# Optimization experiments

Hardware: AMD Instinct MI355X
Metric: run time of the kernel (lower is better)

Reference implementation:

```python
import jax, jax.numpy as jnp
import numpy as np

B, T, D = 8, 1024, 1024
H = 16
DH = D // H  # 64


def setup_inputs() -> dict:
    key = jax.random.key(0)
    k1, k2, k3 = jax.random.split(key, 3)
    x = jax.random.normal(k1, (B, T, D), dtype=jnp.float32)
    W_qkv = jax.random.normal(k2, (3 * D, D), dtype=jnp.float32) * (D ** -0.5)
    W_proj = jax.random.normal(k3, (D, D), dtype=jnp.float32) * (D ** -0.5)
    return {"x": x, "W_qkv": W_qkv, "W_proj": W_proj}


def reference(x, W_qkv, W_proj):
    b, t, _ = x.shape
    # qkv: [B,T,3*D] -> [B,T,3,H,DH]
    qkv = (x @ W_qkv.T).reshape(b, t, 3, H, DH)
    q, k, v = qkv[:, :, 0], qkv[:, :, 1], qkv[:, :, 2]  # [B,T,H,DH]
    scale = DH ** -0.5
    # scores: [B,H,Tq,Tk]
    scores = jnp.einsum("bqhd,bkhd->bhqk", q, k) * scale
    # NOTE: softmax over dim=-2 (the QUERY axis), as in the original module
    attn = jax.nn.softmax(scores, axis=-2)
    out = jnp.einsum("bhqk,bkhd->bqhd", attn, v).reshape(b, t, D)
    return out @ W_proj.T
```

## Files before the change

### kernel.cpp

```cpp
#include <hip/hip_runtime.h>


typedef __bf16 bf16_t;
typedef __bf16 bf16x8 __attribute__((ext_vector_type(8)));
typedef __bf16 bf16x4 __attribute__((ext_vector_type(4)));
typedef float f32x4 __attribute__((ext_vector_type(4)));
typedef unsigned short u16x8 __attribute__((ext_vector_type(8)));
typedef short s16x4 __attribute__((ext_vector_type(4)));

#define DEV __device__ __forceinline__
#define C2 0.18033688f

DEV void gld_lds16(const bf16_t* g, bf16_t* l) {
  __builtin_amdgcn_global_load_lds(
      (const __attribute__((address_space(1))) unsigned int*)g,
      (__attribute__((address_space(3))) unsigned int*)l, 16, 0, 0);
}

DEV float exp2c(float x) { return __builtin_amdgcn_exp2f(fminf(x, 30.f)); }
DEV float sanit(float v) { return (v == v) ? fminf(fmaxf(v, -1e4f), 1e4f) : 0.f; }

DEV int sw64(int r, int kc) { return r * 64 + (((kc ^ (r + (r >> 3))) & 7) << 3); }
DEV int sw32(int r, int kc) { return r * 32 + (((kc ^ r ^ (r >> 2)) & 3) << 3); }

DEV f32x4 mfma16(bf16x8 a, bf16x8 b, f32x4 c) {
  return __builtin_amdgcn_mfma_f32_16x16x32_bf16(a, b, c, 0, 0, 0);
}

DEV f32x4 mfma16k16(bf16x4 a, bf16x4 b, f32x4 c) {
#if defined(__has_builtin) && __has_builtin(__builtin_amdgcn_mfma_f32_16x16x16bf16_1k)
  union U { bf16x4 h; s16x4 s; };
  U ua, ub;
  ua.h = a;
  ub.h = b;
  return __builtin_amdgcn_mfma_f32_16x16x16bf16_1k(ua.s, ub.s, c, 0, 0, 0);
#else
  f32x4 d;
  asm("v_mfma_f32_16x16x16_bf16 %0, %1, %2, %3"
      : "=v"(d)
      : "v"(a), "v"(b), "v"(c));
  return d;
#endif
}

DEV bf16x4 lo4(bf16x8 v) { return __builtin_shufflevector(v, v, 0, 1, 2, 3); }
DEV bf16x4 hi4(bf16x8 v) { return __builtin_shufflevector(v, v, 4, 5, 6, 7); }

__global__ void detect_dtype(const unsigned short* x, int* flag) {
  __shared__ int smax;
  if (threadIdx.x == 0) smax = 0;
  __syncthreads();
  int m = 0;
  for (int i = threadIdx.x; i < 16384; i += 256) {
    int e = (x[i] >> 7) & 0xFF;
    m = m > e ? m : e;
  }
  atomicMax(&smax, m);
  __syncthreads();
  if (threadIdx.x == 0) *flag = (smax >= 160) ? 1 : 0;
}

__global__ void convert_in(const void* __restrict__ x, const void* __restrict__ wq,
                           const void* __restrict__ wp, bf16_t* __restrict__ xb,
                           bf16_t* __restrict__ wqb, bf16_t* __restrict__ wpb,
                           const int* __restrict__ flag) {
  int i = blockIdx.x * 256 + threadIdx.x;
  const void* src;
  bf16_t* dst;
  int off;
  if (i < 1048576) { src = x; dst = xb; off = i; }
  else if (i < 1441792) { src = wq; dst = wqb; off = i - 1048576; }
  else { src = wp; dst = wpb; off = i - 1441792; }
  if (*flag) {
    const float4* s = (const float4*)src;
    float4 a = s[off * 2], b = s[off * 2 + 1];
    bf16x8 o;
    o[0] = (bf16_t)a.x; o[1] = (bf16_t)a.y; o[2] = (bf16_t)a.z; o[3] = (bf16_t)a.w;
    o[4] = (bf16_t)b.x; o[5] = (bf16_t)b.y; o[6] = (bf16_t)b.z; o[7] = (bf16_t)b.w;
    *(bf16x8*)(dst + (size_t)off * 8) = o;
  } else {
    ((u16x8*)dst)[off] = ((const u16x8*)src)[off];
  }
}

__global__ __launch_bounds__(256, 2)
void gemm_bt(const bf16_t* __restrict__ A, int lda, const bf16_t* __restrict__ B,
             bf16_t* __restrict__ Cb, float* __restrict__ Cf, int ldc,
             int K, const int* __restrict__ f32flag) {
  __shared__ bf16_t sA[128 * 32];
  __shared__ bf16_t sB[128 * 32];
  const int tid = threadIdx.x;
  const int wave = tid >> 6, lane = tid & 63;
  const int l = lane & 15, quad = lane >> 4;
  const int row0 = blockIdx.y * 128, col0 = blockIdx.x * 128;
  const int wm = (wave >> 1) * 64, wn = (wave & 1) * 64;
  f32x4 acc[4][4];
#pragma unroll
  for (int i = 0; i < 4; ++i)
#pragma unroll
    for (int j = 0; j < 4; ++j) acc[i][j] = f32x4{0.f, 0.f, 0.f, 0.f};

  for (int k0 = 0; k0 < K; k0 += 32) {
    __syncthreads();
#pragma unroll
    for (int t = 0; t < 2; ++t) {
      int base = t * 256 + wave * 64;
      int n = base + lane;
      int r = n >> 2;
      int kc = ((n & 3) ^ r ^ (r >> 2)) & 3;
      gld_lds16(A + (size_t)(row0 + r) * lda + k0 + kc * 8, sA + base * 8);
      gld_lds16(B + (size_t)(col0 + r) * K + k0 + kc * 8, sB + base * 8);
    }
    __syncthreads();
    bf16x8 af[4], bfr[4];
#pragma unroll
    for (int i = 0; i < 4; ++i)
      af[i] = *(const bf16x8*)&sA[sw32(wm + i * 16 + l, quad)];
#pragma unroll
    for (int j = 0; j < 4; ++j)
      bfr[j] = *(const bf16x8*)&sB[sw32(wn + j * 16 + l, quad)];
#pragma unroll
    for (int i = 0; i < 4; ++i)
#pragma unroll
      for (int j = 0; j < 4; ++j)
        acc[i][j] = mfma16(af[i], bfr[j], acc[i][j]);
  }
  const bool of32 = (f32flag != nullptr) && (*f32flag != 0);
#pragma unroll
  for (int i = 0; i < 4; ++i) {
    int rr = row0 + wm + i * 16 + quad * 4;
#pragma unroll
    for (int j = 0; j < 4; ++j) {
      int cc = col0 + wn + j * 16 + l;
#pragma unroll
      for (int t = 0; t < 4; ++t) {
        float v = sanit(acc[i][j][t]);
        size_t idx = (size_t)(rr + t) * ldc + cc;
        if (of32) Cf[idx] = v; else Cb[idx] = (bf16_t)v;
      }
    }
  }
}

__global__ __launch_bounds__(256, 4)
void attn_stats(const bf16_t* __restrict__ qkv, bf16_t* __restrict__ Vts) {
  __shared__ bf16_t sK[128 * 64];
  __shared__ bf16_t sV[128 * 64];
  __shared__ float sL[128];
  const int bh = blockIdx.x, kt = blockIdx.y;
  const int b = bh >> 4, h = bh & 15;
  const int tid = threadIdx.x, wave = tid >> 6, lane = tid & 63;
  const int l = lane & 15, quad = lane >> 4;
  const size_t rowK = (size_t)b * 1024 + kt * 128;

#pragma unroll
  for (int t = 0; t < 4; ++t) {
    int base = wave * 256 + t * 64;
    int n = base + lane;
    int r = n >> 3;
    int kc = ((n & 7) ^ (r + (r >> 3))) & 7;
    gld_lds16(qkv + (rowK + r) * 3072 + 2048 + h * 64 + kc * 8, sV + base * 8);
    gld_lds16(qkv + (rowK + r) * 3072 + 1024 + h * 64 + kc * 8, sK + base * 8);
  }
  if (tid < 128) sL[tid] = 0.f;
  __syncthreads();

  float accj[8];
#pragma unroll
  for (int j = 0; j < 8; ++j) accj[j] = 0.f;

  for (int qt = 0; qt < 8; ++qt) {
    bf16x8 aq[2][2];
#pragma unroll
    for (int i = 0; i < 2; ++i)
#pragma unroll
      for (int ks = 0; ks < 2; ++ks)
        aq[i][ks] = *(const bf16x8*)&qkv[((size_t)b * 1024 + qt * 128 + wave * 32 +
                                          i * 16 + l) * 3072 + h * 64 +
                                         (ks * 4 + quad) * 8];
#pragma unroll
    for (int j = 0; j < 8; ++j) {
      f32x4 s0 = {0.f, 0.f, 0.f, 0.f}, s1 = {0.f, 0.f, 0.f, 0.f};
#pragma unroll
      for (int ks = 0; ks < 2; ++ks) {
        bf16x8 bk = *(const bf16x8*)&sK[sw64(j * 16 + l, ks * 4 + quad)];
        s0 = mfma16(aq[0][ks], bk, s0);
        s1 = mfma16(aq[1][ks], bk, s1);
      }
#pragma unroll
      for (int t = 0; t < 4; ++t)
        accj[j] += exp2c(s0[t] * C2) + exp2c(s1[t] * C2);
    }
  }
#pragma unroll
  for (int j = 0; j < 8; ++j) {
    float v = accj[j];
    v += __shfl_xor(v, 16);
    v += __shfl_xor(v, 32);
    if (lane < 16) atomicAdd(&sL[j * 16 + l], v);
  }
  __syncthreads();
  if (tid < 128) sL[tid] = 1.0f / fmaxf(sL[tid], 1e-20f);
  __syncthreads();

#pragma unroll
  for (int t = 0; t < 4; ++t) {
    int u = t * 256 + tid;
    int d = u >> 4, k0 = (u & 15) * 8;
    bf16x8 pk;
#pragma unroll
    for (int i = 0; i < 8; ++i) {
      int kl = (k0 & ~31) | ((i >> 2) << 4) | (((k0 >> 3) & 3) << 2) | (i & 3);
      float v = (float)sV[sw64(kl, d >> 3) + (d & 7)];
      pk[i] = (bf16_t)(v * sL[kl]);
    }
    *(bf16x8*)&Vts[((size_t)bh * 64 + d) * 1024 + kt * 128 + k0] = pk;
  }
}

__global__ __launch_bounds__(256, 4)
void attn_out_k(const bf16_t* __restrict__ qkv, const bf16_t* __restrict__ Vts,
                bf16_t* __restrict__ attn) {
  __shared__ bf16_t sK[2][128 * 64];
  const int bh = blockIdx.x, qt = blockIdx.y;
  const int b = bh >> 4, h = bh & 15;
  const int tid = threadIdx.x, wave = tid >> 6, lane = tid & 63;
  const int l = lane & 15, quad = lane >> 4;
  const bf16_t* qbase = qkv + (size_t)b * 3145728 + h * 64;
  const bf16_t* vbase = Vts + (size_t)bh * 65536;

  bf16x8 bq[2][2];
#pragma unroll
  for (int i = 0; i < 2; ++i)
#pragma unroll
    for (int ks = 0; ks < 2; ++ks)
      bq[i][ks] = *(const bf16x8*)&qbase[(size_t)(qt * 128 + wave * 32 + i * 16 + l) *
                                             3072 + ks * 32 + quad * 8];
  f32x4 o[2][4];
#pragma unroll
  for (int i = 0; i < 2; ++i)
#pragma unroll
    for (int jd = 0; jd < 4; ++jd) o[i][jd] = f32x4{0.f, 0.f, 0.f, 0.f};

#pragma unroll
  for (int t = 0; t < 4; ++t) {
    int base = wave * 256 + t * 64;
    int n = base + lane;
    int r = n >> 3;
    int kc = ((n & 7) ^ (r + (r >> 3))) & 7;
    gld_lds16(qkv + ((size_t)b * 1024 + r) * 3072 + 1024 + h * 64 + kc * 8,
              sK[0] + base * 8);
  }

  for (int kt = 0; kt < 8; ++kt) {
    const int buf = kt & 1;
    __syncthreads();
    if (kt < 7) {
#pragma unroll
      for (int t = 0; t < 4; ++t) {
        int base = wave * 256 + t * 64;
        int n = base + lane;
        int r = n >> 3;
        int kc = ((n & 7) ^ (r + (r >> 3))) & 7;
        gld_lds16(qkv + ((size_t)b * 1024 + (kt + 1) * 128 + r) * 3072 + 1024 +
                      h * 64 + kc * 8,
                  sK[buf ^ 1] + base * 8);
      }
    }
    const bf16_t* sKb = sK[buf];
    const bf16_t* vcol = vbase + kt * 128;

    bf16x8 va[2][4];
#pragma unroll
    for (int pc = 0; pc < 2; ++pc)
#pragma unroll
      for (int jd = 0; jd < 4; ++jd)
        va[pc][jd] = *(const bf16x8*)&vcol[(size_t)(jd * 16 + l) * 1024 +
                                           pc * 32 + quad * 8];

#pragma unroll
    for (int ch = 0; ch < 4; ++ch) {
      const int cur = ch & 1;
      bf16x8 ak[2][2];
#pragma unroll
      for (int kk = 0; kk < 2; ++kk)
#pragma unroll
        for (int ks = 0; ks < 2; ++ks)
          ak[kk][ks] = *(const bf16x8*)&sKb[sw64(ch * 32 + kk * 16 + l,
                                                 ks * 4 + quad)];
#pragma unroll
      for (int i = 0; i < 2; ++i) {
        f32x4 st0 = {0.f, 0.f, 0.f, 0.f}, st1 = {0.f, 0.f, 0.f, 0.f};
        st0 = mfma16(ak[0][0], bq[i][0], st0);
        st0 = mfma16(ak[0][1], bq[i][1], st0);
        st1 = mfma16(ak[1][0], bq[i][0], st1);
        st1 = mfma16(ak[1][1], bq[i][1], st1);
        bf16x4 p0, p1;
#pragma unroll
        for (int t = 0; t < 4; ++t) {
          p0[t] = (bf16_t)exp2c(st0[t] * C2);
          p1[t] = (bf16_t)exp2c(st1[t] * C2);
        }
#pragma unroll
        for (int jd = 0; jd < 4; ++jd) {
          o[i][jd] = mfma16k16(lo4(va[cur][jd]), p0, o[i][jd]);
          o[i][jd] = mfma16k16(hi4(va[cur][jd]), p1, o[i][jd]);
        }
      }
      if (ch < 2) {
#pragma unroll
        for (int jd = 0; jd < 4; ++jd)
          va[cur][jd] = *(const bf16x8*)&vcol[(size_t)(jd * 16 + l) * 1024 +
                                              (ch + 2) * 32 + quad * 8];
      }
    }
  }
#pragma unroll
  for (int i = 0; i < 2; ++i) {
    size_t row = (size_t)b * 1024 + qt * 128 + wave * 32 + i * 16 + l;
#pragma unroll
    for (int jd = 0; jd < 4; ++jd) {
      bf16x4 pk;
#pragma unroll
      for (int t = 0; t < 4; ++t) pk[t] = (bf16_t)sanit(o[i][jd][t]);
      *(bf16x4*)&attn[row * 3072 + h * 64 + jd * 16 + quad * 4] = pk;
    }
  }
}

extern "C" void kernel_launch(void* const* d_in, const int* in_sizes, int n_in,
                              void* d_out, int out_size, void* d_ws, size_t ws_size,
                              hipStream_t stream) {
  (void)in_sizes; (void)n_in; (void)out_size; (void)ws_size;
  char* w = (char*)d_ws;
  bf16_t* qkv = (bf16_t*)w;
  bf16_t* xb = (bf16_t*)(w + 50331648);
  bf16_t* Vts = xb;
  bf16_t* Wqkvb = (bf16_t*)(w + 67108864);
  bf16_t* Wprojb = (bf16_t*)(w + 73400320);
  int* flag = (int*)(w + 75497472);
  bf16_t* attn = qkv + 2048;

  detect_dtype<<<1, 256, 0, stream>>>((const unsigned short*)d_in[0], flag);
  convert_in<<<6144, 256, 0, stream>>>(d_in[0], d_in[1], d_in[2],
                                       xb, Wqkvb, Wprojb, flag);

  gemm_bt<<<dim3(24, 64), 256, 0, stream>>>(xb, 1024, Wqkvb, qkv, nullptr, 3072,
                                            1024, nullptr);
  attn_stats<<<dim3(128, 8), 256, 0, stream>>>(qkv, Vts);
  attn_out_k<<<dim3(128, 8), 256, 0, stream>>>(qkv, Vts, attn);
  gemm_bt<<<dim3(8, 64), 256, 0, stream>>>(attn, 3072, Wprojb, (bf16_t*)d_out,
                                           (float*)d_out, 1024, 1024, flag);
}
```

Before: 320.3 us.

## Stage V tiles in LDS and double query tile per attention block

The attention-output kernel now runs 512 threads per block covering 256 query rows instead of 128, which halves the grid. It also stages the pre-scaled transposed V tile into a swizzled, double-buffered LDS array with async global-to-LDS loads, replacing the direct per-wave global reads of V. This lets more query rows share each K/V tile load and cuts redundant global V traffic. The cost is doubled LDS per block (about 64KB) and fewer blocks, which may limit occupancy and latency hiding.

After: 296.1 us. 7.6% less time.

```diff
diff --git a/kernel.cpp b/kernel.cpp
--- a/kernel.cpp
+++ b/kernel.cpp
@@ -218,10 +218,11 @@
   }
 }
 
-__global__ __launch_bounds__(256, 4)
+__global__ __launch_bounds__(512, 4)
 void attn_out_k(const bf16_t* __restrict__ qkv, const bf16_t* __restrict__ Vts,
                 bf16_t* __restrict__ attn) {
   __shared__ bf16_t sK[2][128 * 64];
+  __shared__ bf16_t sV[2][64 * 128];
   const int bh = blockIdx.x, qt = blockIdx.y;
   const int b = bh >> 4, h = bh & 15;
   const int tid = threadIdx.x, wave = tid >> 6, lane = tid & 63;
@@ -234,7 +235,7 @@
   for (int i = 0; i < 2; ++i)
 #pragma unroll
     for (int ks = 0; ks < 2; ++ks)
-      bq[i][ks] = *(const bf16x8*)&qbase[(size_t)(qt * 128 + wave * 32 + i * 16 + l) *
+      bq[i][ks] = *(const bf16x8*)&qbase[(size_t)(qt * 256 + wave * 32 + i * 16 + l) *
                                              3072 + ks * 32 + quad * 8];
   f32x4 o[2][4];
 #pragma unroll
@@ -243,13 +244,15 @@
     for (int jd = 0; jd < 4; ++jd) o[i][jd] = f32x4{0.f, 0.f, 0.f, 0.f};
 
 #pragma unroll
-  for (int t = 0; t < 4; ++t) {
-    int base = wave * 256 + t * 64;
-    int n = base + lane;
+  for (int t = 0; t < 2; ++t) {
+    int n = t * 512 + tid;
     int r = n >> 3;
     int kc = ((n & 7) ^ (r + (r >> 3))) & 7;
     gld_lds16(qkv + ((size_t)b * 1024 + r) * 3072 + 1024 + h * 64 + kc * 8,
-              sK[0] + base * 8);
+              sK[0] + n * 8);
+    int d = n >> 4, s = n & 15;
+    int c = s ^ (d & 7);
+    gld_lds16(vbase + (size_t)d * 1024 + c * 8, sV[0] + n * 8);
   }
 
   for (int kt = 0; kt < 8; ++kt) {
@@ -257,30 +260,24 @@
     __syncthreads();
     if (kt < 7) {
 #pragma unroll
-      for (int t = 0; t < 4; ++t) {
-        int base = wave * 256 + t * 64;
-        int n = base + lane;
+      for (int t = 0; t < 2; ++t) {
+        int n = t * 512 + tid;
         int r = n >> 3;
         int kc = ((n & 7) ^ (r + (r >> 3))) & 7;
         gld_lds16(qkv + ((size_t)b * 1024 + (kt + 1) * 128 + r) * 3072 + 1024 +
                       h * 64 + kc * 8,
-                  sK[buf ^ 1] + base * 8);
+                  sK[buf ^ 1] + n * 8);
+        int d = n >> 4, s = n & 15;
+        int c = s ^ (d & 7);
+        gld_lds16(vbase + (size_t)d * 1024 + (kt + 1) * 128 + c * 8,
+                  sV[buf ^ 1] + n * 8);
       }
     }
     const bf16_t* sKb = sK[buf];
-    const bf16_t* vcol = vbase + kt * 128;
-
-    bf16x8 va[2][4];
-#pragma unroll
-    for (int pc = 0; pc < 2; ++pc)
-#pragma unroll
-      for (int jd = 0; jd < 4; ++jd)
-        va[pc][jd] = *(const bf16x8*)&vcol[(size_t)(jd * 16 + l) * 1024 +
-                                           pc * 32 + quad * 8];
+    const bf16_t* sVb = sV[buf];
 
 #pragma unroll
     for (int ch = 0; ch < 4; ++ch) {
-      const int cur = ch & 1;
       bf16x8 ak[2][2];
 #pragma unroll
       for (int kk = 0; kk < 2; ++kk)
@@ -288,6 +285,11 @@
         for (int ks = 0; ks < 2; ++ks)
           ak[kk][ks] = *(const bf16x8*)&sKb[sw64(ch * 32 + kk * 16 + l,
                                                  ks * 4 + quad)];
+      bf16x8 va[4];
+#pragma unroll
+      for (int jd = 0; jd < 4; ++jd)
+        va[jd] = *(const bf16x8*)&sVb[(jd * 16 + l) * 128 +
+                                      (((ch * 4 + quad) ^ (l & 7)) << 3)];
 #pragma unroll
       for (int i = 0; i < 2; ++i) {
         f32x4 st0 = {0.f, 0.f, 0.f, 0.f}, st1 = {0.f, 0.f, 0.f, 0.f};
@@ -303,21 +305,15 @@
         }
 #pragma unroll
         for (int jd = 0; jd < 4; ++jd) {
-          o[i][jd] = mfma16k16(lo4(va[cur][jd]), p0, o[i][jd]);
-          o[i][jd] = mfma16k16(hi4(va[cur][jd]), p1, o[i][jd]);
+          o[i][jd] = mfma16k16(lo4(va[jd]), p0, o[i][jd]);
+          o[i][jd] = mfma16k16(hi4(va[jd]), p1, o[i][jd]);
         }
       }
-      if (ch < 2) {
-#pragma unroll
-        for (int jd = 0; jd < 4; ++jd)
-          va[cur][jd] = *(const bf16x8*)&vcol[(size_t)(jd * 16 + l) * 1024 +
-                                              (ch + 2) * 32 + quad * 8];
-      }
     }
   }
 #pragma unroll
   for (int i = 0; i < 2; ++i) {
-    size_t row = (size_t)b * 1024 + qt * 128 + wave * 32 + i * 16 + l;
+    size_t row = (size_t)b * 1024 + qt * 256 + wave * 32 + i * 16 + l;
 #pragma unroll
     for (int jd = 0; jd < 4; ++jd) {
       bf16x4 pk;
@@ -348,7 +344,7 @@
   gemm_bt<<<dim3(24, 64), 256, 0, stream>>>(xb, 1024, Wqkvb, qkv, nullptr, 3072,
                                             1024, nullptr);
   attn_stats<<<dim3(128, 8), 256, 0, stream>>>(qkv, Vts);
-  attn_out_k<<<dim3(128, 8), 256, 0, stream>>>(qkv, Vts, attn);
+  attn_out_k<<<dim3(128, 4), 512, 0, stream>>>(qkv, Vts, attn);
   gemm_bt<<<dim3(8, 64), 256, 0, stream>>>(attn, 3072, Wprojb, (bf16_t*)d_out,
                                            (float*)d_out, 1024, 1024, flag);
 }
```
